# Optimization experiments

Measured on AMD Instinct MI355X. Metric: run time of the kernel, lower is better.

Reference implementation:

```python
import jax, jax.numpy as jnp
import numpy as np

N, E, F, H = 50000, 160000, 512, 32
EPS = 1e-5  # BatchNorm eps


def setup_inputs() -> dict:
    key = jax.random.key(0)
    ks = jax.random.split(key, 16)
    s = lambda fan: 1.0 / np.sqrt(fan)
    inp = {
        "x": jax.random.normal(ks[0], (N, 2), jnp.float32),
        "edge_index": jax.random.randint(ks[1], (2, E), 0, N, jnp.int64),
        "face": jax.random.normal(ks[2], (N, F), jnp.float32),
        # encoder: Linear(2,32) -> BN(32) -> PReLU -> Dropout(0) -> Linear(32,32)
        "W1": jax.random.uniform(ks[3], (2, H), jnp.float32, -s(2), s(2)),
        "b1": jnp.zeros((H,), jnp.float32),
        "gamma": jnp.ones((H,), jnp.float32),
        "beta": jnp.zeros((H,), jnp.float32),
        "alpha": jnp.full((1,), 0.25, jnp.float32),  # PReLU default
        "W2": jax.random.uniform(ks[4], (H, H), jnp.float32, -s(H), s(H)),
        "b2": jnp.zeros((H,), jnp.float32),
        "w0": jax.random.uniform(ks[5], (H, 1), jnp.float32, -s(H), s(H)),
        "b0": jnp.zeros((1,), jnp.float32),
        "Wg": jax.random.uniform(ks[6], (H, H), jnp.float32, -s(H), s(H)),
        "bg": jnp.zeros((H,), jnp.float32),
        "wf": jax.random.uniform(ks[7], (H, 1), jnp.float32, -s(H), s(H)),
        "bf": jnp.zeros((1,), jnp.float32),
    }
    return inp


def _encoder(x, W1, b1, gamma, beta, alpha, W2, b2):
    h = x @ W1 + b1
    mu = h.mean(0)
    var = h.var(0)  # biased, matching torch BN training math
    h = (h - mu) * jax.lax.rsqrt(var + EPS) * gamma + beta
    h = jnp.where(h >= 0, h, alpha * h)  # PReLU
    return h @ W2 + b2  # dropout p=0


def _gcn_face(h, edge_index, face, Wg, bg):
    # Face-similarity weighted GCN: w_ij = cos(face_i, face_j),
    # symmetric normalization with self loops (weight 1).
    src, dst = edge_index[0], edge_index[1]
    fn = face * jax.lax.rsqrt(jnp.sum(face * face, axis=1, keepdims=True) + 1e-12)
    ew = jnp.sum(fn[src] * fn[dst], axis=-1)  # [E]
    n = h.shape[0]
    deg = jax.ops.segment_sum(ew, dst, num_segments=n) + 1.0  # + self loop
    norm = ew * jax.lax.rsqrt(deg[src] * deg[dst])  # [E]
    agg = jax.ops.segment_sum(norm[:, None] * h[src], dst, num_segments=n)
    agg = agg + h / deg[:, None]  # self-loop term 1/deg_i
    return agg @ Wg + bg


def reference(x, edge_index, face, W1, b1, gamma, beta, alpha, W2, b2,
              w0, b0, Wg, bg, wf, bf):
    emb = _encoder(x, W1, b1, gamma, beta, alpha, W2, b2)      # [N,32]
    gcn = _gcn_face(emb, edge_index, face, Wg, bg)             # [N,32]
    linear_scores = (emb @ w0 + b0).squeeze(-1)                # [N]
    gcn_scores = (gcn @ wf + bf).squeeze(-1)                   # [N]
    return linear_scores + gcn_scores
```

## Files before the change

kernel.cpp:

```cpp
#include <hip/hip_runtime.h>

#define EPS_BN 1e-5f
#define FDIM 512
#define F4   128
#define HDIM 32
#define NB_XS 64

__device__ __forceinline__ int dot4i8(unsigned a, unsigned b) {
#if __has_builtin(__builtin_amdgcn_sdot4)
    return __builtin_amdgcn_sdot4((int)a, (int)b, 0, false);
#else
    int s;
    s  = (int)(signed char)(a      ) * (int)(signed char)(b      );
    s += (int)(signed char)(a >>  8) * (int)(signed char)(b >>  8);
    s += (int)(signed char)(a >> 16) * (int)(signed char)(b >> 16);
    s += (int)(signed char)(a >> 24) * (int)(signed char)(b >> 24);
    return s;
#endif
}

__global__ __launch_bounds__(256)
void k_prep(const float* __restrict__ face,
            const float* __restrict__ x,
            uint2* __restrict__ qrows,
            float* __restrict__ scales,
            float* __restrict__ deg,
            float* __restrict__ xs,
            int n, int qb) {
    int tid = threadIdx.x;
    if ((int)blockIdx.x < qb) {
        int row  = (int)((blockIdx.x * 256 + tid) >> 6);
        int lane = tid & 63;
        if (row >= n) return;
        const float4* f4 = (const float4*)face + (size_t)row * F4;
        float4 a = f4[lane];
        float4 b = f4[lane + 64];
        float ss = a.x*a.x + a.y*a.y + a.z*a.z + a.w*a.w
                 + b.x*b.x + b.y*b.y + b.z*b.z + b.w*b.w;
        float mx = fmaxf(fmaxf(fmaxf(fabsf(a.x), fabsf(a.y)),
                               fmaxf(fabsf(a.z), fabsf(a.w))),
                         fmaxf(fmaxf(fabsf(b.x), fabsf(b.y)),
                               fmaxf(fabsf(b.z), fabsf(b.w))));
        #pragma unroll
        for (int off = 32; off > 0; off >>= 1) {
            ss += __shfl_xor(ss, off);
            mx  = fmaxf(mx, __shfl_xor(mx, off));
        }
        float rn = rsqrtf(ss + 1e-12f);
        float qs = (mx > 0.f) ? 127.0f / mx : 0.f;
        unsigned da =  ((unsigned)(__float2int_rn(a.x*qs) & 255))
                    | (((unsigned)(__float2int_rn(a.y*qs) & 255)) << 8)
                    | (((unsigned)(__float2int_rn(a.z*qs) & 255)) << 16)
                    | (((unsigned)(__float2int_rn(a.w*qs) & 255)) << 24);
        unsigned db =  ((unsigned)(__float2int_rn(b.x*qs) & 255))
                    | (((unsigned)(__float2int_rn(b.y*qs) & 255)) << 8)
                    | (((unsigned)(__float2int_rn(b.z*qs) & 255)) << 16)
                    | (((unsigned)(__float2int_rn(b.w*qs) & 255)) << 24);
        qrows[(size_t)row * 64 + lane] = make_uint2(da, db);
        if (lane == 0) {
            scales[row] = mx * rn * (1.0f / 127.0f);
            deg[row]    = 0.f;
        }
    } else {
        __shared__ float red[4][5];
        int bid = (int)blockIdx.x - qb;
        float s0=0.f, s1=0.f, s00=0.f, s01=0.f, s11=0.f;
        for (int i = bid * 256 + tid; i < n; i += NB_XS * 256) {
            float2 xv = ((const float2*)x)[i];
            s0  += xv.x;       s1  += xv.y;
            s00 += xv.x*xv.x;  s01 += xv.x*xv.y;  s11 += xv.y*xv.y;
        }
        #pragma unroll
        for (int off = 32; off > 0; off >>= 1) {
            s0  += __shfl_xor(s0,  off);
            s1  += __shfl_xor(s1,  off);
            s00 += __shfl_xor(s00, off);
            s01 += __shfl_xor(s01, off);
            s11 += __shfl_xor(s11, off);
        }
        int lane = tid & 63, w = tid >> 6;
        if (lane == 0) {
            red[w][0]=s0; red[w][1]=s1; red[w][2]=s00; red[w][3]=s01; red[w][4]=s11;
        }
        __syncthreads();
        if (tid < 5) {
            atomicAdd(&xs[tid],
                      red[0][tid] + red[1][tid] + red[2][tid] + red[3][tid]);
        }
    }
}

__global__ __launch_bounds__(256)
void k_main(const float* __restrict__ x,
            const float* __restrict__ W1, const float* __restrict__ b1,
            const float* __restrict__ gamma, const float* __restrict__ beta,
            const float* __restrict__ alpha,
            const float* __restrict__ W2, const float* __restrict__ b2,
            const float* __restrict__ w0,
            const float* __restrict__ Wg, const float* __restrict__ bg,
            const float* __restrict__ wf,
            const float* __restrict__ b0, const float* __restrict__ bf,
            const float* __restrict__ xs,
            const uint4* __restrict__ qrows,
            const float* __restrict__ scales,
            const int* __restrict__ src, const int* __restrict__ dst,
            float* __restrict__ ew,
            float* __restrict__ deg,
            float* __restrict__ sarr,
            float* __restrict__ out,
            int n, int ne, int nbn) {
    if ((int)blockIdx.x < nbn) {
        __shared__ float sW2[HDIM*HDIM];
        __shared__ float sW1[2*HDIM], sb1[HDIM], sa[HDIM], sbsh[HDIM];
        __shared__ float sv[HDIM], sw0[HDIM], sb2[HDIM];
        __shared__ float sc, salpha;
        int tid = threadIdx.x;
        for (int i = tid; i < HDIM*HDIM; i += blockDim.x) sW2[i] = W2[i];
        if (tid < 2*HDIM) sW1[tid] = W1[tid];
        if (tid < HDIM) {
            float invN = 1.0f / (float)n;
            float m0 = xs[0]*invN, m1 = xs[1]*invN;
            float c00 = xs[2]*invN - m0*m0;
            float c01 = xs[3]*invN - m0*m1;
            float c11 = xs[4]*invN - m1*m1;
            float w0j = W1[tid], w1j = W1[HDIM + tid];
            float mu  = m0*w0j + m1*w1j + b1[tid];
            float var = c00*w0j*w0j + 2.f*c01*w0j*w1j + c11*w1j*w1j;
            float aa  = gamma[tid] * rsqrtf(var + EPS_BN);
            sa[tid]   = aa;
            sbsh[tid] = beta[tid] - mu*aa;
            float v = 0.f;
            for (int m = 0; m < HDIM; ++m) v += Wg[tid*HDIM + m] * wf[m];
            sv[tid]  = v;
            sb1[tid] = b1[tid];
            sw0[tid] = w0[tid];
            sb2[tid] = b2[tid];
        } else if (tid == HDIM) {
            float c = b0[0] + bf[0];
            for (int m = 0; m < HDIM; ++m) c += bg[m] * wf[m];
            sc = c;
            salpha = alpha[0];
        }
        __syncthreads();
        int i = blockIdx.x * blockDim.x + tid;
        if (i >= n) return;
        float2 xv = ((const float2*)x)[i];
        float h[HDIM];
        #pragma unroll
        for (int j = 0; j < HDIM; ++j) {
            float t = xv.x*sW1[j] + xv.y*sW1[HDIM + j] + sb1[j];
            t = sa[j]*t + sbsh[j];
            h[j] = (t >= 0.f) ? t : salpha*t;
        }
        float em[HDIM];
        #pragma unroll
        for (int k = 0; k < HDIM; ++k) em[k] = sb2[k];
        #pragma unroll
        for (int j = 0; j < HDIM; ++j) {
            float hj = h[j];
            #pragma unroll
            for (int k = 0; k < HDIM; ++k) em[k] += hj * sW2[j*HDIM + k];
        }
        float sdot = 0.f, ldot = 0.f;
        #pragma unroll
        for (int k = 0; k < HDIM; ++k) { sdot += em[k]*sv[k]; ldot += em[k]*sw0[k]; }
        sarr[i] = sdot;
        out[i]  = ldot + sc;
    } else {
        int e  = ((int)blockIdx.x - nbn) * 32 + (int)(threadIdx.x >> 3);
        int gl = threadIdx.x & 7;
        if (e >= ne) return;
        int si = src[e], di = dst[e];
        const uint4* rs = qrows + (size_t)si * 32;
        const uint4* rd = qrows + (size_t)di * 32;
        uint4 a0 = rs[gl], a1 = rs[gl+8], a2 = rs[gl+16], a3 = rs[gl+24];
        uint4 b0 = rd[gl], b1 = rd[gl+8], b2 = rd[gl+16], b3 = rd[gl+24];
        int acc = dot4i8(a0.x,b0.x) + dot4i8(a0.y,b0.y) + dot4i8(a0.z,b0.z) + dot4i8(a0.w,b0.w)
                + dot4i8(a1.x,b1.x) + dot4i8(a1.y,b1.y) + dot4i8(a1.z,b1.z) + dot4i8(a1.w,b1.w)
                + dot4i8(a2.x,b2.x) + dot4i8(a2.y,b2.y) + dot4i8(a2.z,b2.z) + dot4i8(a2.w,b2.w)
                + dot4i8(a3.x,b3.x) + dot4i8(a3.y,b3.y) + dot4i8(a3.z,b3.z) + dot4i8(a3.w,b3.w);
        acc += __shfl_xor(acc, 4);
        acc += __shfl_xor(acc, 2);
        acc += __shfl_xor(acc, 1);
        if (gl == 0) {
            float w = (float)acc * scales[si] * scales[di];
            ew[e] = w;
            atomicAdd(&deg[di], w);
        }
    }
}

__global__ void k_finish(const int* __restrict__ src,
                         const int* __restrict__ dst,
                         const float* __restrict__ ew,
                         const float* __restrict__ deg,
                         const float* __restrict__ sarr,
                         float* __restrict__ out, int ne, int n) {
    int t = blockIdx.x * blockDim.x + threadIdx.x;
    if (t < ne) {
        int si = src[t], di = dst[t];
        float w = ew[t] * rsqrtf((deg[si] + 1.f) * (deg[di] + 1.f)) * sarr[si];
        atomicAdd(&out[di], w);
    } else if (t < ne + n) {
        int i = t - ne;
        atomicAdd(&out[i], sarr[i] / (deg[i] + 1.f));
    }
}

extern "C" void kernel_launch(void* const* d_in, const int* in_sizes, int n_in,
                              void* d_out, int out_size, void* d_ws, size_t ws_size,
                              hipStream_t stream) {
    const float* x     = (const float*)d_in[0];
    const int*   ei    = (const int*)  d_in[1];
    const float* face  = (const float*)d_in[2];
    const float* W1    = (const float*)d_in[3];
    const float* b1    = (const float*)d_in[4];
    const float* gamma = (const float*)d_in[5];
    const float* beta  = (const float*)d_in[6];
    const float* alpha = (const float*)d_in[7];
    const float* W2    = (const float*)d_in[8];
    const float* b2    = (const float*)d_in[9];
    const float* w0    = (const float*)d_in[10];
    const float* b0    = (const float*)d_in[11];
    const float* Wg    = (const float*)d_in[12];
    const float* bg    = (const float*)d_in[13];
    const float* wf    = (const float*)d_in[14];
    const float* bf    = (const float*)d_in[15];

    const int n  = in_sizes[0] / 2;
    const int ne = in_sizes[1] / 2;
    const int* src = ei;
    const int* dst = ei + ne;

    float* ws     = (float*)d_ws;
    uint2* qrows  = (uint2*)ws;
    float* after  = ws + (size_t)n * 128;
    float* deg    = after;
    float* scales = after + n;
    float* sarr   = after + 2*(size_t)n;
    float* ew     = after + 3*(size_t)n;
    float* xs     = after + 3*(size_t)n + ne;
    float* out    = (float*)d_out;

    const int qb  = (n + 3) / 4;
    const int nbn = (n + 255) / 256;
    const int ebk = (ne + 31) / 32;

    hipMemsetAsync(xs, 0, 8 * sizeof(float), stream);

    k_prep<<<qb + NB_XS, 256, 0, stream>>>(face, x, qrows, scales, deg, xs,
                                           n, qb);

    k_main<<<nbn + ebk, 256, 0, stream>>>(x, W1, b1, gamma, beta, alpha,
                                          W2, b2, w0, Wg, bg, wf, b0, bf, xs,
                                          (const uint4*)qrows, scales,
                                          src, dst, ew, deg, sarr, out,
                                          n, ne, nbn);

    k_finish<<<(ne + n + 255) / 256, 256, 0, stream>>>(src, dst, ew, deg,
                                                       sarr, out, ne, n);
}
```

Measured before the change: 65.52 us.

## Bucket edges by destination block and remap edge blocks across XCDs

```diff
diff --git a/kernel.cpp b/kernel.cpp
--- a/kernel.cpp
+++ b/kernel.cpp
@@ -5,6 +5,10 @@
 #define F4   128
 #define HDIM 32
 #define NB_XS 64
+#define NSC   64
+#define CAP   320
+#define OVFCAP 4096
+#define OVB   8
 
 __device__ __forceinline__ int dot4i8(unsigned a, unsigned b) {
 #if __has_builtin(__builtin_amdgcn_sdot4)
@@ -19,51 +23,45 @@
 #endif
 }
 
+__device__ __forceinline__ unsigned bkt_of(unsigned slot) {
+    return ((slot >> 6) * 52429u) >> 18;
+}
+
 __global__ __launch_bounds__(256)
 void k_prep(const float* __restrict__ face,
             const float* __restrict__ x,
+            const int* __restrict__ src,
+            const int* __restrict__ dst,
             uint2* __restrict__ qrows,
             float* __restrict__ scales,
             float* __restrict__ deg,
             float* __restrict__ xs,
-            int n, int qb) {
+            int*   __restrict__ cnt,
+            int*   __restrict__ ovfc,
+            unsigned* __restrict__ se,
+            unsigned* __restrict__ ovf,
+            int n, int ne) {
     int tid = threadIdx.x;
-    if ((int)blockIdx.x < qb) {
-        int row  = (int)((blockIdx.x * 256 + tid) >> 6);
-        int lane = tid & 63;
-        if (row >= n) return;
-        const float4* f4 = (const float4*)face + (size_t)row * F4;
-        float4 a = f4[lane];
-        float4 b = f4[lane + 64];
-        float ss = a.x*a.x + a.y*a.y + a.z*a.z + a.w*a.w
-                 + b.x*b.x + b.y*b.y + b.z*b.z + b.w*b.w;
-        float mx = fmaxf(fmaxf(fmaxf(fabsf(a.x), fabsf(a.y)),
-                               fmaxf(fabsf(a.z), fabsf(a.w))),
-                         fmaxf(fmaxf(fabsf(b.x), fabsf(b.y)),
-                               fmaxf(fabsf(b.z), fabsf(b.w))));
-        #pragma unroll
-        for (int off = 32; off > 0; off >>= 1) {
-            ss += __shfl_xor(ss, off);
-            mx  = fmaxf(mx, __shfl_xor(mx, off));
-        }
-        float rn = rsqrtf(ss + 1e-12f);
-        float qs = (mx > 0.f) ? 127.0f / mx : 0.f;
-        unsigned da =  ((unsigned)(__float2int_rn(a.x*qs) & 255))
-                    | (((unsigned)(__float2int_rn(a.y*qs) & 255)) << 8)
-                    | (((unsigned)(__float2int_rn(a.z*qs) & 255)) << 16)
-                    | (((unsigned)(__float2int_rn(a.w*qs) & 255)) << 24);
-        unsigned db =  ((unsigned)(__float2int_rn(b.x*qs) & 255))
-                    | (((unsigned)(__float2int_rn(b.y*qs) & 255)) << 8)
-                    | (((unsigned)(__float2int_rn(b.z*qs) & 255)) << 16)
-                    | (((unsigned)(__float2int_rn(b.w*qs) & 255)) << 24);
-        qrows[(size_t)row * 64 + lane] = make_uint2(da, db);
-        if (lane == 0) {
-            scales[row] = mx * rn * (1.0f / 127.0f);
-            deg[row]    = 0.f;
-        }
-    } else {
+
+    if ((int)blockIdx.x < NSC) {
+        for (int e = (int)blockIdx.x * 256 + tid; e < ne; e += NSC * 256) {
+            unsigned s = (unsigned)src[e], d = (unsigned)dst[e];
+            unsigned b = d >> 6;
+            int pos = atomicAdd(&cnt[b], 1);
+            unsigned u = (d << 16) | s;
+            if (pos < CAP) {
+                se[b * CAP + pos] = u;
+            } else {
+                int o = atomicAdd(ovfc, 1);
+                if (o < OVFCAP) ovf[o] = u;
+            }
+        }
+        return;
+    }
+
+    if ((int)blockIdx.x < NSC + NB_XS) {
         __shared__ float red[4][5];
-        int bid = (int)blockIdx.x - qb;
+        int bid = (int)blockIdx.x - NSC;
         float s0=0.f, s1=0.f, s00=0.f, s01=0.f, s11=0.f;
         for (int i = bid * 256 + tid; i < n; i += NB_XS * 256) {
             float2 xv = ((const float2*)x)[i];
@@ -83,10 +81,43 @@
             red[w][0]=s0; red[w][1]=s1; red[w][2]=s00; red[w][3]=s01; red[w][4]=s11;
         }
         __syncthreads();
-        if (tid < 5) {
+        if (tid < 5)
             atomicAdd(&xs[tid],
                       red[0][tid] + red[1][tid] + red[2][tid] + red[3][tid]);
-        }
+        return;
+    }
+
+    int row  = (int)(((blockIdx.x - NSC - NB_XS) * 256 + tid) >> 6);
+    int lane = tid & 63;
+    if (row >= n) return;
+    const float4* f4 = (const float4*)face + (size_t)row * F4;
+    float4 a = f4[lane];
+    float4 b = f4[lane + 64];
+    float ss = a.x*a.x + a.y*a.y + a.z*a.z + a.w*a.w
+             + b.x*b.x + b.y*b.y + b.z*b.z + b.w*b.w;
+    float mx = fmaxf(fmaxf(fmaxf(fabsf(a.x), fabsf(a.y)),
+                           fmaxf(fabsf(a.z), fabsf(a.w))),
+                     fmaxf(fmaxf(fabsf(b.x), fabsf(b.y)),
+                           fmaxf(fabsf(b.z), fabsf(b.w))));
+    #pragma unroll
+    for (int off = 32; off > 0; off >>= 1) {
+        ss += __shfl_xor(ss, off);
+        mx  = fmaxf(mx, __shfl_xor(mx, off));
+    }
+    float rn = rsqrtf(ss + 1e-12f);
+    float qs = (mx > 0.f) ? 127.0f / mx : 0.f;
+    unsigned da =  ((unsigned)(__float2int_rn(a.x*qs) & 255))
+                | (((unsigned)(__float2int_rn(a.y*qs) & 255)) << 8)
+                | (((unsigned)(__float2int_rn(a.z*qs) & 255)) << 16)
+                | (((unsigned)(__float2int_rn(a.w*qs) & 255)) << 24);
+    unsigned db =  ((unsigned)(__float2int_rn(b.x*qs) & 255))
+                | (((unsigned)(__float2int_rn(b.y*qs) & 255)) << 8)
+                | (((unsigned)(__float2int_rn(b.z*qs) & 255)) << 16)
+                | (((unsigned)(__float2int_rn(b.w*qs) & 255)) << 24);
+    qrows[(size_t)row * 64 + lane] = make_uint2(da, db);
+    if (lane == 0) {
+        scales[row] = mx * rn * (1.0f / 127.0f);
+        deg[row]    = 0.f;
     }
 }
 
@@ -103,18 +134,23 @@
             const float* __restrict__ xs,
             const uint4* __restrict__ qrows,
             const float* __restrict__ scales,
-            const int* __restrict__ src, const int* __restrict__ dst,
+            const unsigned* __restrict__ se,
+            const int* __restrict__ cnt,
+            const unsigned* __restrict__ ovf,
+            const int* __restrict__ ovfc,
             float* __restrict__ ew,
+            float* __restrict__ ew_ovf,
             float* __restrict__ deg,
             float* __restrict__ sarr,
             float* __restrict__ out,
-            int n, int ne, int nbn) {
+            int n, int nbn, int nbn8, int ebk, int nslots) {
+    int tid = threadIdx.x;
+
     if ((int)blockIdx.x < nbn) {
         __shared__ float sW2[HDIM*HDIM];
         __shared__ float sW1[2*HDIM], sb1[HDIM], sa[HDIM], sbsh[HDIM];
         __shared__ float sv[HDIM], sw0[HDIM], sb2[HDIM];
         __shared__ float sc, salpha;
-        int tid = threadIdx.x;
         for (int i = tid; i < HDIM*HDIM; i += blockDim.x) sW2[i] = W2[i];
         if (tid < 2*HDIM) sW1[tid] = W1[tid];
         if (tid < HDIM) {
@@ -166,11 +202,24 @@
         for (int k = 0; k < HDIM; ++k) { sdot += em[k]*sv[k]; ldot += em[k]*sw0[k]; }
         sarr[i] = sdot;
         out[i]  = ldot + sc;
-    } else {
-        int e  = ((int)blockIdx.x - nbn) * 32 + (int)(threadIdx.x >> 3);
-        int gl = threadIdx.x & 7;
-        if (e >= ne) return;
-        int si = src[e], di = dst[e];
+        return;
+    }
+    if ((int)blockIdx.x < nbn8) return;
+
+    if ((int)blockIdx.x < nbn8 + ebk) {
+        int h   = (int)blockIdx.x - nbn8;
+        int q   = ebk >> 3, r = ebk & 7;
+        int xcd = h & 7, idx = h >> 3;
+        int blk = (xcd < r) ? xcd*(q+1) + idx : r*(q+1) + (xcd-r)*q + idx;
+
+        int slot = blk * 32 + (tid >> 3);
+        int gl   = tid & 7;
+        unsigned b = bkt_of((unsigned)slot);
+        int ix = slot - (int)b * CAP;
+        int c  = cnt[b]; if (c > CAP) c = CAP;
+        if (ix >= c) return;
+        unsigned u = se[slot];
+        int si = (int)(u & 0xFFFFu), di = (int)(u >> 16);
         const uint4* rs = qrows + (size_t)si * 32;
         const uint4* rd = qrows + (size_t)di * 32;
         uint4 a0 = rs[gl], a1 = rs[gl+8], a2 = rs[gl+16], a3 = rs[gl+24];
@@ -184,26 +233,69 @@
         acc += __shfl_xor(acc, 1);
         if (gl == 0) {
             float w = (float)acc * scales[si] * scales[di];
-            ew[e] = w;
+            ew[slot] = w;
             atomicAdd(&deg[di], w);
         }
-    }
-}
-
-__global__ void k_finish(const int* __restrict__ src,
-                         const int* __restrict__ dst,
+        return;
+    }
+
+    {
+        int obid = (int)blockIdx.x - nbn8 - ebk;
+        int ovn = *ovfc; if (ovn > OVFCAP) ovn = OVFCAP;
+        int gl  = tid & 7;
+        for (int e = obid * 32 + (tid >> 3); e < ovn; e += OVB * 32) {
+            unsigned u = ovf[e];
+            int si = (int)(u & 0xFFFFu), di = (int)(u >> 16);
+            const uint4* rs = qrows + (size_t)si * 32;
+            const uint4* rd = qrows + (size_t)di * 32;
+            uint4 a0 = rs[gl], a1 = rs[gl+8], a2 = rs[gl+16], a3 = rs[gl+24];
+            uint4 b0 = rd[gl], b1 = rd[gl+8], b2 = rd[gl+16], b3 = rd[gl+24];
+            int acc = dot4i8(a0.x,b0.x) + dot4i8(a0.y,b0.y) + dot4i8(a0.z,b0.z) + dot4i8(a0.w,b0.w)
+                    + dot4i8(a1.x,b1.x) + dot4i8(a1.y,b1.y) + dot4i8(a1.z,b1.z) + dot4i8(a1.w,b1.w)
+                    + dot4i8(a2.x,b2.x) + dot4i8(a2.y,b2.y) + dot4i8(a2.z,b2.z) + dot4i8(a2.w,b2.w)
+                    + dot4i8(a3.x,b3.x) + dot4i8(a3.y,b3.y) + dot4i8(a3.z,b3.z) + dot4i8(a3.w,b3.w);
+            acc += __shfl_xor(acc, 4);
+            acc += __shfl_xor(acc, 2);
+            acc += __shfl_xor(acc, 1);
+            if (gl == 0) {
+                float w = (float)acc * scales[si] * scales[di];
+                ew_ovf[e] = w;
+                atomicAdd(&deg[di], w);
+            }
+        }
+    }
+}
+
+__global__ void k_finish(const unsigned* __restrict__ se,
+                         const int* __restrict__ cnt,
                          const float* __restrict__ ew,
+                         const unsigned* __restrict__ ovf,
+                         const int* __restrict__ ovfc,
+                         const float* __restrict__ ew_ovf,
                          const float* __restrict__ deg,
                          const float* __restrict__ sarr,
-                         float* __restrict__ out, int ne, int n) {
+                         float* __restrict__ out, int nslots, int n) {
     int t = blockIdx.x * blockDim.x + threadIdx.x;
-    if (t < ne) {
-        int si = src[t], di = dst[t];
+    if (t < nslots) {
+        unsigned b = bkt_of((unsigned)t);
+        int ix = t - (int)b * CAP;
+        int c  = cnt[b]; if (c > CAP) c = CAP;
+        if (ix >= c) return;
+        unsigned u = se[t];
+        int si = (int)(u & 0xFFFFu), di = (int)(u >> 16);
         float w = ew[t] * rsqrtf((deg[si] + 1.f) * (deg[di] + 1.f)) * sarr[si];
         atomicAdd(&out[di], w);
-    } else if (t < ne + n) {
-        int i = t - ne;
+    } else if (t < nslots + n) {
+        int i = t - nslots;
         atomicAdd(&out[i], sarr[i] / (deg[i] + 1.f));
+    } else {
+        int o = t - nslots - n;
+        int ovn = *ovfc; if (ovn > OVFCAP) ovn = OVFCAP;
+        if (o >= ovn) return;
+        unsigned u = ovf[o];
+        int si = (int)(u & 0xFFFFu), di = (int)(u >> 16);
+        float w = ew_ovf[o] * rsqrtf((deg[si] + 1.f) * (deg[di] + 1.f)) * sarr[si];
+        atomicAdd(&out[di], w);
     }
 }
 
@@ -232,31 +324,39 @@
     const int* src = ei;
     const int* dst = ei + ne;
 
-    float* ws     = (float*)d_ws;
-    uint2* qrows  = (uint2*)ws;
-    float* after  = ws + (size_t)n * 128;
-    float* deg    = after;
-    float* scales = after + n;
-    float* sarr   = after + 2*(size_t)n;
-    float* ew     = after + 3*(size_t)n;
-    float* xs     = after + 3*(size_t)n + ne;
-    float* out    = (float*)d_out;
-
-    const int qb  = (n + 3) / 4;
-    const int nbn = (n + 255) / 256;
-    const int ebk = (ne + 31) / 32;
-
-    hipMemsetAsync(xs, 0, 8 * sizeof(float), stream);
-
-    k_prep<<<qb + NB_XS, 256, 0, stream>>>(face, x, qrows, scales, deg, xs,
-                                           n, qb);
-
-    k_main<<<nbn + ebk, 256, 0, stream>>>(x, W1, b1, gamma, beta, alpha,
-                                          W2, b2, w0, Wg, bg, wf, b0, bf, xs,
-                                          (const uint4*)qrows, scales,
-                                          src, dst, ew, deg, sarr, out,
-                                          n, ne, nbn);
-
-    k_finish<<<(ne + n + 255) / 256, 256, 0, stream>>>(src, dst, ew, deg,
-                                                       sarr, out, ne, n);
-}
+    const int nbkt   = (n + 63) >> 6;
+    const int nslots = nbkt * CAP;
+
+    float*    ws     = (float*)d_ws;
+    uint2*    qrows  = (uint2*)ws;
+    float*    after  = ws + (size_t)n * 128;
+    float*    deg    = after;
+    float*    scales = after + n;
+    float*    sarr   = after + 2*(size_t)n;
+    float*    xs     = after + 3*(size_t)n;
+    int*      cnt    = (int*)(xs + 8);
+    int*      ovfc   = cnt + 1024;
+    unsigned* se     = (unsigned*)(ovfc + 8);
+    float*    ew     = (float*)(se + nslots);
+    unsigned* ovf    = (unsigned*)(ew + nslots);
+    float*    ew_ovf = (float*)(ovf + OVFCAP);
+    float*    out    = (float*)d_out;
+
+    const int qb   = (n + 3) / 4;
+    const int nbn  = (n + 255) / 256;
+    const int nbn8 = (nbn + 7) & ~7;
+    const int ebk  = (nslots + 31) / 32;
+
+    hipMemsetAsync(xs, 0, (8 + 1024 + 8) * sizeof(float), stream);
+
+    k_prep<<<NSC + NB_XS + qb, 256, 0, stream>>>(
+        face, x, src, dst, qrows, scales, deg, xs, cnt, ovfc, se, ovf, n, ne);
+
+    k_main<<<nbn8 + ebk + OVB, 256, 0, stream>>>(
+        x, W1, b1, gamma, beta, alpha, W2, b2, w0, Wg, bg, wf, b0, bf, xs,
+        (const uint4*)qrows, scales, se, cnt, ovf, ovfc, ew, ew_ovf,
+        deg, sarr, out, n, nbn, nbn8, ebk, nslots);
+
+    k_finish<<<(nslots + n + OVFCAP + 255) / 256, 256, 0, stream>>>(
+        se, cnt, ew, ovf, ovfc, ew_ovf, deg, sarr, out, nslots, n);
+}
```

After: 81.28 us. 1.24x slower.

## Fuse three launches into one cooperative persistent kernel with grid syncs

Applied to the files above, without the earlier changes.

```diff
diff --git a/kernel.cpp b/kernel.cpp
--- a/kernel.cpp
+++ b/kernel.cpp
@@ -1,10 +1,14 @@
 #include <hip/hip_runtime.h>
+#include <hip/hip_cooperative_groups.h>
+
+namespace cg = cooperative_groups;
 
 #define EPS_BN 1e-5f
 #define FDIM 512
 #define F4   128
 #define HDIM 32
 #define NB_XS 64
+#define GB_MAX 1024
 
 __device__ __forceinline__ int dot4i8(unsigned a, unsigned b) {
 #if __has_builtin(__builtin_amdgcn_sdot4)
@@ -19,19 +23,19 @@
 #endif
 }
 
-__global__ __launch_bounds__(256)
-void k_prep(const float* __restrict__ face,
-            const float* __restrict__ x,
-            uint2* __restrict__ qrows,
-            float* __restrict__ scales,
-            float* __restrict__ deg,
-            float* __restrict__ xs,
-            int n, int qb) {
-    int tid = threadIdx.x;
-    if ((int)blockIdx.x < qb) {
-        int row  = (int)((blockIdx.x * 256 + tid) >> 6);
-        int lane = tid & 63;
-        if (row >= n) return;
+struct NodeSmem {
+    float W2[HDIM*HDIM];
+    float W1[2*HDIM], b1v[HDIM], a[HDIM], bsh[HDIM];
+    float v[HDIM], w0v[HDIM], b2v[HDIM];
+    float c, alpha;
+    float xsl[5];
+};
+
+__device__ __forceinline__
+void quant_rows(const float* __restrict__ face, uint2* __restrict__ qrows,
+                float* __restrict__ scales, float* __restrict__ deg,
+                int n, int wid0, int wstride, int lane) {
+    for (int row = wid0; row < n; row += wstride) {
         const float4* f4 = (const float4*)face + (size_t)row * F4;
         float4 a = f4[lane];
         float4 b = f4[lane + 64];
@@ -61,124 +65,131 @@
             scales[row] = mx * rn * (1.0f / 127.0f);
             deg[row]    = 0.f;
         }
-    } else {
-        __shared__ float red[4][5];
-        int bid = (int)blockIdx.x - qb;
-        float s0=0.f, s1=0.f, s00=0.f, s01=0.f, s11=0.f;
-        for (int i = bid * 256 + tid; i < n; i += NB_XS * 256) {
-            float2 xv = ((const float2*)x)[i];
-            s0  += xv.x;       s1  += xv.y;
-            s00 += xv.x*xv.x;  s01 += xv.x*xv.y;  s11 += xv.y*xv.y;
-        }
-        #pragma unroll
-        for (int off = 32; off > 0; off >>= 1) {
-            s0  += __shfl_xor(s0,  off);
-            s1  += __shfl_xor(s1,  off);
-            s00 += __shfl_xor(s00, off);
-            s01 += __shfl_xor(s01, off);
-            s11 += __shfl_xor(s11, off);
-        }
-        int lane = tid & 63, w = tid >> 6;
-        if (lane == 0) {
-            red[w][0]=s0; red[w][1]=s1; red[w][2]=s00; red[w][3]=s01; red[w][4]=s11;
-        }
-        __syncthreads();
-        if (tid < 5) {
-            atomicAdd(&xs[tid],
-                      red[0][tid] + red[1][tid] + red[2][tid] + red[3][tid]);
-        }
-    }
-}
-
-__global__ __launch_bounds__(256)
-void k_main(const float* __restrict__ x,
-            const float* __restrict__ W1, const float* __restrict__ b1,
-            const float* __restrict__ gamma, const float* __restrict__ beta,
-            const float* __restrict__ alpha,
-            const float* __restrict__ W2, const float* __restrict__ b2,
-            const float* __restrict__ w0,
-            const float* __restrict__ Wg, const float* __restrict__ bg,
-            const float* __restrict__ wf,
-            const float* __restrict__ b0, const float* __restrict__ bf,
-            const float* __restrict__ xs,
-            const uint4* __restrict__ qrows,
-            const float* __restrict__ scales,
-            const int* __restrict__ src, const int* __restrict__ dst,
-            float* __restrict__ ew,
-            float* __restrict__ deg,
-            float* __restrict__ sarr,
-            float* __restrict__ out,
-            int n, int ne, int nbn) {
-    if ((int)blockIdx.x < nbn) {
-        __shared__ float sW2[HDIM*HDIM];
-        __shared__ float sW1[2*HDIM], sb1[HDIM], sa[HDIM], sbsh[HDIM];
-        __shared__ float sv[HDIM], sw0[HDIM], sb2[HDIM];
-        __shared__ float sc, salpha;
-        int tid = threadIdx.x;
-        for (int i = tid; i < HDIM*HDIM; i += blockDim.x) sW2[i] = W2[i];
-        if (tid < 2*HDIM) sW1[tid] = W1[tid];
-        if (tid < HDIM) {
-            float invN = 1.0f / (float)n;
-            float m0 = xs[0]*invN, m1 = xs[1]*invN;
-            float c00 = xs[2]*invN - m0*m0;
-            float c01 = xs[3]*invN - m0*m1;
-            float c11 = xs[4]*invN - m1*m1;
-            float w0j = W1[tid], w1j = W1[HDIM + tid];
-            float mu  = m0*w0j + m1*w1j + b1[tid];
-            float var = c00*w0j*w0j + 2.f*c01*w0j*w1j + c11*w1j*w1j;
-            float aa  = gamma[tid] * rsqrtf(var + EPS_BN);
-            sa[tid]   = aa;
-            sbsh[tid] = beta[tid] - mu*aa;
-            float v = 0.f;
-            for (int m = 0; m < HDIM; ++m) v += Wg[tid*HDIM + m] * wf[m];
-            sv[tid]  = v;
-            sb1[tid] = b1[tid];
-            sw0[tid] = w0[tid];
-            sb2[tid] = b2[tid];
-        } else if (tid == HDIM) {
-            float c = b0[0] + bf[0];
-            for (int m = 0; m < HDIM; ++m) c += bg[m] * wf[m];
-            sc = c;
-            salpha = alpha[0];
-        }
-        __syncthreads();
-        int i = blockIdx.x * blockDim.x + tid;
-        if (i >= n) return;
+    }
+}
+
+__device__ __forceinline__
+void xsums_block(const float* __restrict__ x, float* __restrict__ part,
+                 int n, int xbid, int tid) {
+    __shared__ float red[4][5];
+    float s0=0.f, s1=0.f, s00=0.f, s01=0.f, s11=0.f;
+    for (int i = xbid * 256 + tid; i < n; i += NB_XS * 256) {
+        float2 xv = ((const float2*)x)[i];
+        s0  += xv.x;       s1  += xv.y;
+        s00 += xv.x*xv.x;  s01 += xv.x*xv.y;  s11 += xv.y*xv.y;
+    }
+    #pragma unroll
+    for (int off = 32; off > 0; off >>= 1) {
+        s0  += __shfl_xor(s0,  off);
+        s1  += __shfl_xor(s1,  off);
+        s00 += __shfl_xor(s00, off);
+        s01 += __shfl_xor(s01, off);
+        s11 += __shfl_xor(s11, off);
+    }
+    int lane = tid & 63, w = tid >> 6;
+    if (lane == 0) {
+        red[w][0]=s0; red[w][1]=s1; red[w][2]=s00; red[w][3]=s01; red[w][4]=s11;
+    }
+    __syncthreads();
+    if (tid < 5)
+        part[xbid * 5 + tid] = red[0][tid] + red[1][tid]
+                             + red[2][tid] + red[3][tid];
+}
+
+__device__ __forceinline__
+void node_work(NodeSmem* s, const float* __restrict__ x,
+               const float* __restrict__ W1, const float* __restrict__ b1,
+               const float* __restrict__ gamma, const float* __restrict__ beta,
+               const float* __restrict__ alpha,
+               const float* __restrict__ W2, const float* __restrict__ b2,
+               const float* __restrict__ w0,
+               const float* __restrict__ Wg, const float* __restrict__ bg,
+               const float* __restrict__ wf,
+               const float* __restrict__ b0, const float* __restrict__ bf,
+               const float* __restrict__ part,
+               float* __restrict__ sarr, float* __restrict__ out,
+               int n, int tid, int c0, int cstride) {
+    for (int i = tid; i < HDIM*HDIM; i += 256) s->W2[i] = W2[i];
+    if (tid < 2*HDIM) s->W1[tid] = W1[tid];
+    if (tid < 5) {
+        float acc = 0.f;
+        for (int i = 0; i < NB_XS; ++i) acc += part[i * 5 + tid];
+        s->xsl[tid] = acc;
+    }
+    __syncthreads();
+    if (tid < HDIM) {
+        float invN = 1.0f / (float)n;
+        float m0 = s->xsl[0]*invN, m1 = s->xsl[1]*invN;
+        float c00 = s->xsl[2]*invN - m0*m0;
+        float c01 = s->xsl[3]*invN - m0*m1;
+        float c11 = s->xsl[4]*invN - m1*m1;
+        float w0j = W1[tid], w1j = W1[HDIM + tid];
+        float mu  = m0*w0j + m1*w1j + b1[tid];
+        float var = c00*w0j*w0j + 2.f*c01*w0j*w1j + c11*w1j*w1j;
+        float aa  = gamma[tid] * rsqrtf(var + EPS_BN);
+        s->a[tid]   = aa;
+        s->bsh[tid] = beta[tid] - mu*aa;
+        float v = 0.f;
+        for (int m = 0; m < HDIM; ++m) v += Wg[tid*HDIM + m] * wf[m];
+        s->v[tid]   = v;
+        s->b1v[tid] = b1[tid];
+        s->w0v[tid] = w0[tid];
+        s->b2v[tid] = b2[tid];
+    } else if (tid == HDIM) {
+        float c = b0[0] + bf[0];
+        for (int m = 0; m < HDIM; ++m) c += bg[m] * wf[m];
+        s->c = c;
+        s->alpha = alpha[0];
+    }
+    __syncthreads();
+    const int nbn = (n + 255) >> 8;
+    for (int cb = c0; cb < nbn; cb += cstride) {
+        int i = cb * 256 + tid;
+        if (i >= n) continue;
         float2 xv = ((const float2*)x)[i];
         float h[HDIM];
         #pragma unroll
         for (int j = 0; j < HDIM; ++j) {
-            float t = xv.x*sW1[j] + xv.y*sW1[HDIM + j] + sb1[j];
-            t = sa[j]*t + sbsh[j];
-            h[j] = (t >= 0.f) ? t : salpha*t;
+            float t = xv.x*s->W1[j] + xv.y*s->W1[HDIM + j] + s->b1v[j];
+            t = s->a[j]*t + s->bsh[j];
+            h[j] = (t >= 0.f) ? t : s->alpha*t;
         }
         float em[HDIM];
         #pragma unroll
-        for (int k = 0; k < HDIM; ++k) em[k] = sb2[k];
+        for (int k = 0; k < HDIM; ++k) em[k] = s->b2v[k];
         #pragma unroll
         for (int j = 0; j < HDIM; ++j) {
             float hj = h[j];
             #pragma unroll
-            for (int k = 0; k < HDIM; ++k) em[k] += hj * sW2[j*HDIM + k];
+            for (int k = 0; k < HDIM; ++k) em[k] += hj * s->W2[j*HDIM + k];
         }
         float sdot = 0.f, ldot = 0.f;
         #pragma unroll
-        for (int k = 0; k < HDIM; ++k) { sdot += em[k]*sv[k]; ldot += em[k]*sw0[k]; }
+        for (int k = 0; k < HDIM; ++k) {
+            sdot += em[k]*s->v[k]; ldot += em[k]*s->w0v[k];
+        }
         sarr[i] = sdot;
-        out[i]  = ldot + sc;
-    } else {
-        int e  = ((int)blockIdx.x - nbn) * 32 + (int)(threadIdx.x >> 3);
-        int gl = threadIdx.x & 7;
-        if (e >= ne) return;
+        out[i]  = ldot + s->c;
+    }
+}
+
+__device__ __forceinline__
+void edge_work(const uint4* __restrict__ rows, const float* __restrict__ scales,
+               const int* __restrict__ src, const int* __restrict__ dst,
+               float* __restrict__ ew, float* __restrict__ deg,
+               int ne, int e0, int estride, int gl) {
+    for (int e = e0; e < ne; e += estride) {
         int si = src[e], di = dst[e];
-        const uint4* rs = qrows + (size_t)si * 32;
-        const uint4* rd = qrows + (size_t)di * 32;
-        uint4 a0 = rs[gl], a1 = rs[gl+8], a2 = rs[gl+16], a3 = rs[gl+24];
-        uint4 b0 = rd[gl], b1 = rd[gl+8], b2 = rd[gl+16], b3 = rd[gl+24];
-        int acc = dot4i8(a0.x,b0.x) + dot4i8(a0.y,b0.y) + dot4i8(a0.z,b0.z) + dot4i8(a0.w,b0.w)
-                + dot4i8(a1.x,b1.x) + dot4i8(a1.y,b1.y) + dot4i8(a1.z,b1.z) + dot4i8(a1.w,b1.w)
-                + dot4i8(a2.x,b2.x) + dot4i8(a2.y,b2.y) + dot4i8(a2.z,b2.z) + dot4i8(a2.w,b2.w)
-                + dot4i8(a3.x,b3.x) + dot4i8(a3.y,b3.y) + dot4i8(a3.z,b3.z) + dot4i8(a3.w,b3.w);
+        const uint4* rs = rows + (size_t)si * 32;
+        const uint4* rd = rows + (size_t)di * 32;
+        uint4 A0 = rs[gl],      B0 = rd[gl];
+        uint4 A1 = rs[gl + 8],  B1 = rd[gl + 8];
+        uint4 A2 = rs[gl + 16], B2 = rd[gl + 16];
+        uint4 A3 = rs[gl + 24], B3 = rd[gl + 24];
+        int acc = dot4i8(A0.x,B0.x) + dot4i8(A0.y,B0.y) + dot4i8(A0.z,B0.z) + dot4i8(A0.w,B0.w)
+                + dot4i8(A1.x,B1.x) + dot4i8(A1.y,B1.y) + dot4i8(A1.z,B1.z) + dot4i8(A1.w,B1.w)
+                + dot4i8(A2.x,B2.x) + dot4i8(A2.y,B2.y) + dot4i8(A2.z,B2.z) + dot4i8(A2.w,B2.w)
+                + dot4i8(A3.x,B3.x) + dot4i8(A3.y,B3.y) + dot4i8(A3.z,B3.z) + dot4i8(A3.w,B3.w);
         acc += __shfl_xor(acc, 4);
         acc += __shfl_xor(acc, 2);
         acc += __shfl_xor(acc, 1);
@@ -190,73 +201,182 @@
     }
 }
 
-__global__ void k_finish(const int* __restrict__ src,
-                         const int* __restrict__ dst,
-                         const float* __restrict__ ew,
-                         const float* __restrict__ deg,
-                         const float* __restrict__ sarr,
-                         float* __restrict__ out, int ne, int n) {
-    int t = blockIdx.x * blockDim.x + threadIdx.x;
-    if (t < ne) {
-        int si = src[t], di = dst[t];
-        float w = ew[t] * rsqrtf((deg[si] + 1.f) * (deg[di] + 1.f)) * sarr[si];
-        atomicAdd(&out[di], w);
-    } else if (t < ne + n) {
-        int i = t - ne;
-        atomicAdd(&out[i], sarr[i] / (deg[i] + 1.f));
-    }
+__device__ __forceinline__
+void finish_work(const int* __restrict__ src, const int* __restrict__ dst,
+                 const float* __restrict__ ew, const float* __restrict__ deg,
+                 const float* __restrict__ sarr, float* __restrict__ out,
+                 int ne, int n, int t0, int tstride) {
+    for (int t = t0; t < ne + n; t += tstride) {
+        if (t < ne) {
+            int si = src[t], di = dst[t];
+            float w = ew[t] * rsqrtf((deg[si] + 1.f) * (deg[di] + 1.f)) * sarr[si];
+            atomicAdd(&out[di], w);
+        } else {
+            int i = t - ne;
+            atomicAdd(&out[i], sarr[i] / (deg[i] + 1.f));
+        }
+    }
+}
+
+__global__ __launch_bounds__(256, 4)
+void k_fused(const float* __restrict__ face, const float* __restrict__ x,
+             const int* __restrict__ src, const int* __restrict__ dst,
+             const float* __restrict__ W1, const float* __restrict__ b1,
+             const float* __restrict__ gamma, const float* __restrict__ beta,
+             const float* __restrict__ alpha,
+             const float* __restrict__ W2, const float* __restrict__ b2,
+             const float* __restrict__ w0,
+             const float* __restrict__ Wg, const float* __restrict__ bg,
+             const float* __restrict__ wf,
+             const float* __restrict__ b0, const float* __restrict__ bf,
+             uint2* __restrict__ qrows, float* __restrict__ scales,
+             float* __restrict__ deg, float* __restrict__ part,
+             float* __restrict__ ew, float* __restrict__ sarr,
+             float* __restrict__ out, int n, int ne) {
+    cg::grid_group grid = cg::this_grid();
+    const int tid = threadIdx.x;
+    const int bid = (int)blockIdx.x;
+    const int gb  = (int)gridDim.x;
+    __shared__ NodeSmem ns;
+
+    quant_rows(face, qrows, scales, deg, n, bid*4 + (tid>>6), gb*4, tid & 63);
+    if (bid < NB_XS) xsums_block(x, part, n, bid, tid);
+
+    grid.sync();
+
+    const int nbn   = (n + 255) >> 8;
+    const int rnode = (nbn < (gb >> 2)) ? nbn : (gb >> 2);
+    if (bid < rnode) {
+        node_work(&ns, x, W1, b1, gamma, beta, alpha, W2, b2, w0,
+                  Wg, bg, wf, b0, bf, part, sarr, out, n, tid, bid, rnode);
+    } else {
+        edge_work((const uint4*)qrows, scales, src, dst, ew, deg, ne,
+                  (bid - rnode)*32 + (tid >> 3), (gb - rnode)*32, tid & 7);
+    }
+
+    grid.sync();
+
+    finish_work(src, dst, ew, deg, sarr, out, ne, n, bid*256 + tid, gb*256);
+}
+
+__global__ __launch_bounds__(256)
+void k_pA(const float* __restrict__ face, const float* __restrict__ x,
+          uint2* __restrict__ qrows, float* __restrict__ scales,
+          float* __restrict__ deg, float* __restrict__ part, int n, int qb) {
+    int tid = threadIdx.x, bid = (int)blockIdx.x;
+    if (bid < qb)
+        quant_rows(face, qrows, scales, deg, n, bid*4 + (tid>>6), qb*4, tid & 63);
+    else
+        xsums_block(x, part, n, bid - qb, tid);
+}
+
+__global__ __launch_bounds__(256)
+void k_pB(const float* __restrict__ x,
+          const float* __restrict__ W1, const float* __restrict__ b1,
+          const float* __restrict__ gamma, const float* __restrict__ beta,
+          const float* __restrict__ alpha,
+          const float* __restrict__ W2, const float* __restrict__ b2,
+          const float* __restrict__ w0,
+          const float* __restrict__ Wg, const float* __restrict__ bg,
+          const float* __restrict__ wf,
+          const float* __restrict__ b0, const float* __restrict__ bf,
+          const float* __restrict__ part,
+          const uint2* __restrict__ qrows, const float* __restrict__ scales,
+          const int* __restrict__ src, const int* __restrict__ dst,
+          float* __restrict__ ew, float* __restrict__ deg,
+          float* __restrict__ sarr, float* __restrict__ out, int n, int ne) {
+    int tid = threadIdx.x, bid = (int)blockIdx.x;
+    const int nbn = (n + 255) >> 8;
+    __shared__ NodeSmem ns;
+    if (bid < nbn) {
+        node_work(&ns, x, W1, b1, gamma, beta, alpha, W2, b2, w0,
+                  Wg, bg, wf, b0, bf, part, sarr, out, n, tid, bid, nbn);
+    } else {
+        edge_work((const uint4*)qrows, scales, src, dst, ew, deg, ne,
+                  (bid - nbn)*32 + (tid >> 3),
+                  ((int)gridDim.x - nbn)*32, tid & 7);
+    }
+}
+
+__global__ __launch_bounds__(256)
+void k_pC(const int* __restrict__ src, const int* __restrict__ dst,
+          const float* __restrict__ ew, const float* __restrict__ deg,
+          const float* __restrict__ sarr, float* __restrict__ out,
+          int ne, int n) {
+    finish_work(src, dst, ew, deg, sarr, out, ne, n,
+                (int)blockIdx.x*256 + (int)threadIdx.x,
+                (int)gridDim.x*256);
 }
 
 extern "C" void kernel_launch(void* const* d_in, const int* in_sizes, int n_in,
                               void* d_out, int out_size, void* d_ws, size_t ws_size,
                               hipStream_t stream) {
-    const float* x     = (const float*)d_in[0];
-    const int*   ei    = (const int*)  d_in[1];
-    const float* face  = (const float*)d_in[2];
-    const float* W1    = (const float*)d_in[3];
-    const float* b1    = (const float*)d_in[4];
-    const float* gamma = (const float*)d_in[5];
-    const float* beta  = (const float*)d_in[6];
-    const float* alpha = (const float*)d_in[7];
-    const float* W2    = (const float*)d_in[8];
-    const float* b2    = (const float*)d_in[9];
-    const float* w0    = (const float*)d_in[10];
-    const float* b0    = (const float*)d_in[11];
-    const float* Wg    = (const float*)d_in[12];
-    const float* bg    = (const float*)d_in[13];
-    const float* wf    = (const float*)d_in[14];
-    const float* bf    = (const float*)d_in[15];
-
-    const int n  = in_sizes[0] / 2;
-    const int ne = in_sizes[1] / 2;
-    const int* src = ei;
-    const int* dst = ei + ne;
-
-    float* ws     = (float*)d_ws;
-    uint2* qrows  = (uint2*)ws;
-    float* after  = ws + (size_t)n * 128;
-    float* deg    = after;
-    float* scales = after + n;
-    float* sarr   = after + 2*(size_t)n;
-    float* ew     = after + 3*(size_t)n;
-    float* xs     = after + 3*(size_t)n + ne;
-    float* out    = (float*)d_out;
-
-    const int qb  = (n + 3) / 4;
-    const int nbn = (n + 255) / 256;
-    const int ebk = (ne + 31) / 32;
-
-    hipMemsetAsync(xs, 0, 8 * sizeof(float), stream);
-
-    k_prep<<<qb + NB_XS, 256, 0, stream>>>(face, x, qrows, scales, deg, xs,
-                                           n, qb);
-
-    k_main<<<nbn + ebk, 256, 0, stream>>>(x, W1, b1, gamma, beta, alpha,
-                                          W2, b2, w0, Wg, bg, wf, b0, bf, xs,
-                                          (const uint4*)qrows, scales,
-                                          src, dst, ew, deg, sarr, out,
-                                          n, ne, nbn);
-
-    k_finish<<<(ne + n + 255) / 256, 256, 0, stream>>>(src, dst, ew, deg,
-                                                       sarr, out, ne, n);
-}
+    const float* x_p     = (const float*)d_in[0];
+    const int*   ei      = (const int*)  d_in[1];
+    const float* face_p  = (const float*)d_in[2];
+    const float* W1_p    = (const float*)d_in[3];
+    const float* b1_p    = (const float*)d_in[4];
+    const float* gamma_p = (const float*)d_in[5];
+    const float* beta_p  = (const float*)d_in[6];
+    const float* alpha_p = (const float*)d_in[7];
+    const float* W2_p    = (const float*)d_in[8];
+    const float* b2_p    = (const float*)d_in[9];
+    const float* w0_p    = (const float*)d_in[10];
+    const float* b0_p    = (const float*)d_in[11];
+    const float* Wg_p    = (const float*)d_in[12];
+    const float* bg_p    = (const float*)d_in[13];
+    const float* wf_p    = (const float*)d_in[14];
+    const float* bf_p    = (const float*)d_in[15];
+
+    int n  = in_sizes[0] / 2;
+    int ne = in_sizes[1] / 2;
+    const int* src_p = ei;
+    const int* dst_p = ei + ne;
+
+    float*  ws       = (float*)d_ws;
+    uint2*  qrows_p  = (uint2*)ws;
+    float*  after    = ws + (size_t)n * 128;
+    float*  deg_p    = after;
+    float*  scales_p = after + n;
+    float*  sarr_p   = after + 2*(size_t)n;
+    float*  ew_p     = after + 3*(size_t)n;
+    float*  part_p   = after + 3*(size_t)n + ne;
+    float*  out_p    = (float*)d_out;
+
+    int maxBlocksPerCU = 0;
+    hipError_t qerr = hipOccupancyMaxActiveBlocksPerMultiprocessor(
+        &maxBlocksPerCU, k_fused, 256, 0);
+    int gb = (qerr == hipSuccess) ? maxBlocksPerCU * 256 : 0;
+    if (gb > GB_MAX) gb = GB_MAX;
+
+    hipError_t lerr = hipErrorUnknown;
+    if (gb >= 256) {
+        void* args[] = {
+            (void*)&face_p, (void*)&x_p, (void*)&src_p, (void*)&dst_p,
+            (void*)&W1_p, (void*)&b1_p, (void*)&gamma_p, (void*)&beta_p,
+            (void*)&alpha_p, (void*)&W2_p, (void*)&b2_p, (void*)&w0_p,
+            (void*)&Wg_p, (void*)&bg_p, (void*)&wf_p, (void*)&b0_p,
+            (void*)&bf_p, (void*)&qrows_p, (void*)&scales_p, (void*)&deg_p,
+            (void*)&part_p, (void*)&ew_p, (void*)&sarr_p, (void*)&out_p,
+            (void*)&n, (void*)&ne
+        };
+        lerr = hipLaunchCooperativeKernel((void*)k_fused, dim3(gb), dim3(256),
+                                          args, 0, stream);
+    }
+
+    if (lerr != hipSuccess) {
+        const int qb  = (n + 3) / 4;
+        const int nbn = (n + 255) / 256;
+        const int ebk = (ne + 31) / 32;
+        k_pA<<<qb + NB_XS, 256, 0, stream>>>(face_p, x_p, qrows_p, scales_p,
+                                             deg_p, part_p, n, qb);
+        k_pB<<<nbn + ebk, 256, 0, stream>>>(x_p, W1_p, b1_p, gamma_p, beta_p,
+                                            alpha_p, W2_p, b2_p, w0_p, Wg_p,
+                                            bg_p, wf_p, b0_p, bf_p, part_p,
+                                            qrows_p, scales_p, src_p, dst_p,
+                                            ew_p, deg_p, sarr_p, out_p, n, ne);
+        k_pC<<<(ne + n + 255) / 256, 256, 0, stream>>>(src_p, dst_p, ew_p,
+                                                       deg_p, sarr_p, out_p,
+                                                       ne, n);
+    }
+}
```

New measurement: 243.9 us. +272.3%, slower.
